# Performance work log

Measured on AMD Instinct MI355X. Metric: run time of the kernel, lower is better.

Reference implementation:

```python
import jax, jax.numpy as jnp
import numpy as np

DIM = 300
SCALES = (1, 2, 4, 10, 25)


def setup_inputs() -> dict:
    key = jax.random.key(0)
    k1, k2, k3 = jax.random.split(key, 3)
    N = 100000  # divisible by all scales -> rest == 0, matching the main path
    inputs_c_e = jax.random.normal(k1, (N, DIM), dtype=jnp.float32)
    Ws = jax.random.normal(k2, (len(SCALES), DIM, DIM), dtype=jnp.float32) * 0.05
    bs = jax.random.normal(k3, (len(SCALES), DIM), dtype=jnp.float32) * 0.05
    return {"inputs_c_e": inputs_c_e, "Ws": Ws, "bs": bs}


def _contract_expand(x, Ws, bs):
    # x: [N, DIM]; for each scale r: segment-sum groups of r rows, relu(Linear),
    # broadcast back (divided by r), then concat all scales along rows.
    N = x.shape[0]
    outs = []
    for i, r in enumerate(SCALES):
        groups = N // r
        rest = N - r * groups
        # sum over each full group of r consecutive rows -> [groups, DIM]
        sums = x[: r * groups].reshape(groups, r, DIM).sum(axis=1)
        if rest != 0:
            tail = x[r * groups :].sum(axis=0) * (r / rest)  # [DIM]
            sums = jnp.concatenate([sums, tail[None, :]], axis=0)
        # PyTorch Linear: y = s @ W.T + b, then relu, then divide by r
        h = jax.nn.relu(sums @ Ws[i].T + bs[i]) / r  # [groups(+1), DIM]
        expanded = jnp.repeat(h[:groups], r, axis=0)  # [r*groups, DIM]
        if rest != 0:
            expanded = jnp.concatenate(
                [expanded, jnp.broadcast_to(h[groups], (rest, DIM))], axis=0
            )
        outs.append(expanded)
    return jnp.concatenate(outs, axis=0)  # [5*N, DIM]


def reference(inputs_c_e, Ws, bs):
    return _contract_expand(inputs_c_e, Ws, bs)
```

## Files before the change

### kernel.cpp

```cpp
#include <hip/hip_runtime.h>
#include <hip/hip_bf16.h>

#define DIM 300

using shortx4 = __attribute__((ext_vector_type(4))) short;
using shortx8 = __attribute__((ext_vector_type(8))) short;
using floatx4 = __attribute__((ext_vector_type(4))) float;

__device__ __forceinline__ short f2bf(float f) {
  union { __hip_bfloat16 h; short s; } u;
  u.h = __float2bfloat16(f);
  return u.s;
}

__global__ void prep_w_kernel(const float* __restrict__ Ws, short* __restrict__ wsB) {
  int t = blockIdx.x * 256 + threadIdx.x;
  if (t >= 5 * 19 * 10 * 64) return;
  int fid = t >> 6, lane = t & 63;
  int s = fid / 190; int rem = fid - s * 190;
  int nt = rem / 10; int kk = rem - nt * 10;
  int n  = nt * 16 + (lane & 15);
  int k0 = kk * 32 + (lane >> 4) * 8;
  shortx8 v;
  #pragma unroll
  for (int j = 0; j < 8; ++j) {
    int k = k0 + j;
    float f = (n < DIM && k < DIM) ? Ws[s * (DIM * DIM) + n * DIM + k] : 0.0f;
    v[j] = f2bf(f);
  }
  *reinterpret_cast<shortx8*>(wsB + (size_t)fid * 512 + lane * 8) = v;
}

template <int R>
__device__ __forceinline__ void run_tile(
    const float* __restrict__ x, const float* __restrict__ bs,
    float* __restrict__ out, const short* __restrict__ wsB,
    int si, int tile, int N, short* A, float* bsh)
{
  const int tid = threadIdx.x;
  const int groups = N / R;
  const int g0 = tile * 64;
  int validM = groups - g0; if (validM > 64) validM = 64;

  for (int t = tid; t < 304; t += 256) bsh[t] = (t < DIM) ? bs[si * DIM + t] : 0.0f;

  for (int idx = tid; idx < 64 * 82; idx += 256) {
    int m  = idx / 82;
    int kv = idx - m * 82;
    float ax = 0.f, ay = 0.f, az = 0.f, aw = 0.f;
    if (kv < 75 && m < validM) {
      const float* p = x + ((size_t)(g0 + m) * R) * DIM + kv * 4;
      #pragma unroll
      for (int j = 0; j < R; ++j) {
        float4 v = *reinterpret_cast<const float4*>(p + j * DIM);
        ax += v.x; ay += v.y; az += v.z; aw += v.w;
      }
    }
    shortx4 h;
    h[0] = f2bf(ax); h[1] = f2bf(ay); h[2] = f2bf(az); h[3] = f2bf(aw);
    *reinterpret_cast<shortx4*>(&A[m * 328 + kv * 4]) = h;
  }
  __syncthreads();

  const int lane = tid & 63;
  const int wave = tid >> 6;
  const int lr   = lane & 15;
  const int quad = lane >> 4;
  const int wm   = wave * 16;

  shortx8 af[10];
  #pragma unroll
  for (int kk = 0; kk < 10; ++kk)
    af[kk] = *reinterpret_cast<const shortx8*>(&A[(wm + lr) * 328 + kk * 32 + quad * 8]);
  __syncthreads();

  short* Stage = A;
  const float inv_r = 1.0f / (float)R;
  const short* wb = wsB + (size_t)si * 190 * 512 + lane * 8;

  #pragma unroll 1
  for (int nt = 0; nt < 19; ++nt) {
    floatx4 acc = {0.f, 0.f, 0.f, 0.f};
    const short* wnt = wb + nt * 10 * 512;
    #pragma unroll
    for (int kk = 0; kk < 10; ++kk) {
      shortx8 bf = *reinterpret_cast<const shortx8*>(wnt + kk * 512);
      acc = __builtin_amdgcn_mfma_f32_16x16x32_bf16(af[kk], bf, acc, 0, 0, 0);
    }
    const int n = nt * 16 + lr;
    const float b = bsh[n];
    #pragma unroll
    for (int j = 0; j < 4; ++j) {
      float v = acc[j] + b;
      v = v > 0.f ? v * inv_r : 0.f;
      Stage[(wm + quad * 4 + j) * 312 + n] = f2bf(v);
    }
  }
  __syncthreads();

  float4* __restrict__ outv =
      reinterpret_cast<float4*>(out) + ((size_t)si * N + (size_t)g0 * R) * 75;
  const int total = validM * R * 75;
  for (int f = tid; f < total; f += 256) {
    int mr = f / 75;
    int c  = f - mr * 75;
    int sm = mr / R;
    int2 d = *reinterpret_cast<const int2*>(&Stage[sm * 312 + c * 4]);
    float4 o;
    o.x = __uint_as_float(((unsigned)d.x) << 16);
    o.y = __uint_as_float(((unsigned)d.x) & 0xffff0000u);
    o.z = __uint_as_float(((unsigned)d.y) << 16);
    o.w = __uint_as_float(((unsigned)d.y) & 0xffff0000u);
    outv[f] = o;
  }
}

__global__ __launch_bounds__(256) void ce_main_kernel(
    const float* __restrict__ x, const float* __restrict__ bs,
    float* __restrict__ out, const short* __restrict__ wsB,
    int N, int b0, int b1, int b2, int b3)
{
  __shared__ __align__(16) short A[64 * 328];
  __shared__ float bsh[304];
  const int bid = blockIdx.x;
  if (bid < b0)      run_tile<25>(x, bs, out, wsB, 4, bid,      N, A, bsh);
  else if (bid < b1) run_tile<10>(x, bs, out, wsB, 3, bid - b0, N, A, bsh);
  else if (bid < b2) run_tile<4> (x, bs, out, wsB, 2, bid - b1, N, A, bsh);
  else if (bid < b3) run_tile<2> (x, bs, out, wsB, 1, bid - b2, N, A, bsh);
  else               run_tile<1> (x, bs, out, wsB, 0, bid - b3, N, A, bsh);
}

extern "C" void kernel_launch(void* const* d_in, const int* in_sizes, int n_in,
                              void* d_out, int out_size, void* d_ws, size_t ws_size,
                              hipStream_t stream) {
  const float* x  = (const float*)d_in[0];
  const float* Ws = (const float*)d_in[1];
  const float* bs = (const float*)d_in[2];
  float* out = (float*)d_out;
  short* wsB = (short*)d_ws;

  const int N = in_sizes[0] / DIM;

  prep_w_kernel<<<(5 * 19 * 10 * 64 + 255) / 256, 256, 0, stream>>>(Ws, wsB);

  const int t25 = (N / 25 + 63) / 64;
  const int t10 = (N / 10 + 63) / 64;
  const int t4  = (N / 4  + 63) / 64;
  const int t2  = (N / 2  + 63) / 64;
  const int t1  = (N      + 63) / 64;
  const int b0 = t25;
  const int b1 = b0 + t10;
  const int b2 = b1 + t4;
  const int b3 = b2 + t2;
  const int total = b3 + t1;

  ce_main_kernel<<<total, 256, 0, stream>>>(x, bs, out, wsB, N, b0, b1, b2, b3);
}
```

Baseline: 800.2 us.

## Split segment-sum into separate kernel writing bf16 rows to workspace

Splits the fused kernel into a sum kernel, which reduces each group of rows to bf16 and writes it to a global workspace, and a GEMM+expand kernel that reads those bf16 rows straight into MFMA fragments. The second kernel needs only the staging buffer in LDS and requests 4 blocks per CU, so it can keep more blocks resident for the write-heavy expand phase. The sum loads also widen to 8 floats per thread. In exchange it adds an extra launch and a workspace round trip, and it falls back to the old kernel if the workspace is too small.

```diff
diff --git a/kernel.cpp b/kernel.cpp
--- a/kernel.cpp
+++ b/kernel.cpp
@@ -32,35 +32,65 @@
 }
 
 template <int R>
-__device__ __forceinline__ void run_tile(
-    const float* __restrict__ x, const float* __restrict__ bs,
-    float* __restrict__ out, const short* __restrict__ wsB,
-    int si, int tile, int N, short* A, float* bsh)
+__device__ __forceinline__ void sum_tile(
+    const float* __restrict__ x, short* __restrict__ Arow,
+    int tile, int bid, int N)
 {
   const int tid = threadIdx.x;
   const int groups = N / R;
   const int g0 = tile * 64;
   int validM = groups - g0; if (validM > 64) validM = 64;
-
-  for (int t = tid; t < 304; t += 256) bsh[t] = (t < DIM) ? bs[si * DIM + t] : 0.0f;
-
-  for (int idx = tid; idx < 64 * 82; idx += 256) {
-    int m  = idx / 82;
-    int kv = idx - m * 82;
-    float ax = 0.f, ay = 0.f, az = 0.f, aw = 0.f;
-    if (kv < 75 && m < validM) {
-      const float* p = x + ((size_t)(g0 + m) * R) * DIM + kv * 4;
+  short* dst = Arow + (size_t)bid * (64 * 320);
+
+  for (int idx = tid; idx < 64 * 40; idx += 256) {
+    int m  = idx / 40;
+    int ko = idx - m * 40;
+    float a0=0.f,a1=0.f,a2=0.f,a3=0.f,a4=0.f,a5=0.f,a6=0.f,a7=0.f;
+    if (m < validM) {
+      const float* p = x + ((size_t)(g0 + m) * R) * DIM + ko * 8;
+      const bool lo = (ko * 2     < 75);
+      const bool hi = (ko * 2 + 1 < 75);
       #pragma unroll
       for (int j = 0; j < R; ++j) {
-        float4 v = *reinterpret_cast<const float4*>(p + j * DIM);
-        ax += v.x; ay += v.y; az += v.z; aw += v.w;
+        if (lo) {
+          float4 v = *reinterpret_cast<const float4*>(p + j * DIM);
+          a0 += v.x; a1 += v.y; a2 += v.z; a3 += v.w;
+        }
+        if (hi) {
+          float4 v = *reinterpret_cast<const float4*>(p + j * DIM + 4);
+          a4 += v.x; a5 += v.y; a6 += v.z; a7 += v.w;
+        }
       }
     }
-    shortx4 h;
-    h[0] = f2bf(ax); h[1] = f2bf(ay); h[2] = f2bf(az); h[3] = f2bf(aw);
-    *reinterpret_cast<shortx4*>(&A[m * 328 + kv * 4]) = h;
-  }
-  __syncthreads();
+    shortx8 v;
+    v[0]=f2bf(a0); v[1]=f2bf(a1); v[2]=f2bf(a2); v[3]=f2bf(a3);
+    v[4]=f2bf(a4); v[5]=f2bf(a5); v[6]=f2bf(a6); v[7]=f2bf(a7);
+    *reinterpret_cast<shortx8*>(dst + m * 320 + ko * 8) = v;
+  }
+}
+
+__global__ __launch_bounds__(256) void sum_kernel(
+    const float* __restrict__ x, short* __restrict__ Arow,
+    int N, int b0, int b1, int b2, int b3)
+{
+  const int bid = blockIdx.x;
+  if (bid < b0)      sum_tile<25>(x, Arow, bid,      bid, N);
+  else if (bid < b1) sum_tile<10>(x, Arow, bid - b0, bid, N);
+  else if (bid < b2) sum_tile<4> (x, Arow, bid - b1, bid, N);
+  else if (bid < b3) sum_tile<2> (x, Arow, bid - b2, bid, N);
+  else               sum_tile<1> (x, Arow, bid - b3, bid, N);
+}
+
+template <int R>
+__device__ __forceinline__ void run_tile2(
+    const float* __restrict__ bs, float* __restrict__ out,
+    const short* __restrict__ wsB, const short* __restrict__ Arow,
+    int si, int tile, int bid, int N, short* Stage)
+{
+  const int tid = threadIdx.x;
+  const int groups = N / R;
+  const int g0 = tile * 64;
+  int validM = groups - g0; if (validM > 64) validM = 64;
 
   const int lane = tid & 63;
   const int wave = tid >> 6;
@@ -68,13 +98,12 @@
   const int quad = lane >> 4;
   const int wm   = wave * 16;
 
+  const short* arow = Arow + ((size_t)bid * 64 + wm + lr) * 320 + quad * 8;
   shortx8 af[10];
   #pragma unroll
   for (int kk = 0; kk < 10; ++kk)
-    af[kk] = *reinterpret_cast<const shortx8*>(&A[(wm + lr) * 328 + kk * 32 + quad * 8]);
-  __syncthreads();
-
-  short* Stage = A;
+    af[kk] = *reinterpret_cast<const shortx8*>(arow + kk * 32);
+
   const float inv_r = 1.0f / (float)R;
   const short* wb = wsB + (size_t)si * 190 * 512 + lane * 8;
 
@@ -88,7 +117,7 @@
       acc = __builtin_amdgcn_mfma_f32_16x16x32_bf16(af[kk], bf, acc, 0, 0, 0);
     }
     const int n = nt * 16 + lr;
-    const float b = bsh[n];
+    const float b = (n < DIM) ? bs[si * DIM + n] : 0.0f;
     #pragma unroll
     for (int j = 0; j < 4; ++j) {
       float v = acc[j] + b;
@@ -115,6 +144,104 @@
   }
 }
 
+__global__ __launch_bounds__(256, 4) void ce_main2_kernel(
+    const float* __restrict__ bs, float* __restrict__ out,
+    const short* __restrict__ wsB, const short* __restrict__ Arow,
+    int N, int b0, int b1, int b2, int b3)
+{
+  __shared__ __align__(16) short Stage[64 * 312];
+  const int bid = blockIdx.x;
+  if (bid < b0)      run_tile2<25>(bs, out, wsB, Arow, 4, bid,      bid, N, Stage);
+  else if (bid < b1) run_tile2<10>(bs, out, wsB, Arow, 3, bid - b0, bid, N, Stage);
+  else if (bid < b2) run_tile2<4> (bs, out, wsB, Arow, 2, bid - b1, bid, N, Stage);
+  else if (bid < b3) run_tile2<2> (bs, out, wsB, Arow, 1, bid - b2, bid, N, Stage);
+  else               run_tile2<1> (bs, out, wsB, Arow, 0, bid - b3, bid, N, Stage);
+}
+
+template <int R>
+__device__ __forceinline__ void run_tile(
+    const float* __restrict__ x, const float* __restrict__ bs,
+    float* __restrict__ out, const short* __restrict__ wsB,
+    int si, int tile, int N, short* A, float* bsh)
+{
+  const int tid = threadIdx.x;
+  const int groups = N / R;
+  const int g0 = tile * 64;
+  int validM = groups - g0; if (validM > 64) validM = 64;
+
+  for (int t = tid; t < 304; t += 256) bsh[t] = (t < DIM) ? bs[si * DIM + t] : 0.0f;
+
+  for (int idx = tid; idx < 64 * 82; idx += 256) {
+    int m  = idx / 82;
+    int kv = idx - m * 82;
+    float ax = 0.f, ay = 0.f, az = 0.f, aw = 0.f;
+    if (kv < 75 && m < validM) {
+      const float* p = x + ((size_t)(g0 + m) * R) * DIM + kv * 4;
+      #pragma unroll
+      for (int j = 0; j < R; ++j) {
+        float4 v = *reinterpret_cast<const float4*>(p + j * DIM);
+        ax += v.x; ay += v.y; az += v.z; aw += v.w;
+      }
+    }
+    shortx4 h;
+    h[0] = f2bf(ax); h[1] = f2bf(ay); h[2] = f2bf(az); h[3] = f2bf(aw);
+    *reinterpret_cast<shortx4*>(&A[m * 328 + kv * 4]) = h;
+  }
+  __syncthreads();
+
+  const int lane = tid & 63;
+  const int wave = tid >> 6;
+  const int lr   = lane & 15;
+  const int quad = lane >> 4;
+  const int wm   = wave * 16;
+
+  shortx8 af[10];
+  #pragma unroll
+  for (int kk = 0; kk < 10; ++kk)
+    af[kk] = *reinterpret_cast<const shortx8*>(&A[(wm + lr) * 328 + kk * 32 + quad * 8]);
+  __syncthreads();
+
+  short* Stage = A;
+  const float inv_r = 1.0f / (float)R;
+  const short* wb = wsB + (size_t)si * 190 * 512 + lane * 8;
+
+  #pragma unroll 1
+  for (int nt = 0; nt < 19; ++nt) {
+    floatx4 acc = {0.f, 0.f, 0.f, 0.f};
+    const short* wnt = wb + nt * 10 * 512;
+    #pragma unroll
+    for (int kk = 0; kk < 10; ++kk) {
+      shortx8 bf = *reinterpret_cast<const shortx8*>(wnt + kk * 512);
+      acc = __builtin_amdgcn_mfma_f32_16x16x32_bf16(af[kk], bf, acc, 0, 0, 0);
+    }
+    const int n = nt * 16 + lr;
+    const float b = bsh[n];
+    #pragma unroll
+    for (int j = 0; j < 4; ++j) {
+      float v = acc[j] + b;
+      v = v > 0.f ? v * inv_r : 0.f;
+      Stage[(wm + quad * 4 + j) * 312 + n] = f2bf(v);
+    }
+  }
+  __syncthreads();
+
+  float4* __restrict__ outv =
+      reinterpret_cast<float4*>(out) + ((size_t)si * N + (size_t)g0 * R) * 75;
+  const int total = validM * R * 75;
+  for (int f = tid; f < total; f += 256) {
+    int mr = f / 75;
+    int c  = f - mr * 75;
+    int sm = mr / R;
+    int2 d = *reinterpret_cast<const int2*>(&Stage[sm * 312 + c * 4]);
+    float4 o;
+    o.x = __uint_as_float(((unsigned)d.x) << 16);
+    o.y = __uint_as_float(((unsigned)d.x) & 0xffff0000u);
+    o.z = __uint_as_float(((unsigned)d.y) << 16);
+    o.w = __uint_as_float(((unsigned)d.y) & 0xffff0000u);
+    outv[f] = o;
+  }
+}
+
 __global__ __launch_bounds__(256) void ce_main_kernel(
     const float* __restrict__ x, const float* __restrict__ bs,
     float* __restrict__ out, const short* __restrict__ wsB,
@@ -154,5 +281,14 @@
   const int b3 = b2 + t2;
   const int total = b3 + t1;
 
-  ce_main_kernel<<<total, 256, 0, stream>>>(x, bs, out, wsB, N, b0, b1, b2, b3);
-}
+  const size_t wsB_bytes = 972800;
+  const size_t arow_bytes = (size_t)total * 64 * 320 * sizeof(short);
+
+  if (ws_size >= wsB_bytes + arow_bytes) {
+    short* Arow = wsB + wsB_bytes / sizeof(short);
+    sum_kernel<<<total, 256, 0, stream>>>(x, Arow, N, b0, b1, b2, b3);
+    ce_main2_kernel<<<total, 256, 0, stream>>>(bs, out, wsB, Arow, N, b0, b1, b2, b3);
+  } else {
+    ce_main_kernel<<<total, 256, 0, stream>>>(x, bs, out, wsB, N, b0, b1, b2, b3);
+  }
+}
```

New measurement: 916.1 us. 14.5% more time.

## Make each wave own its 16 rows end to end and drop block barriers

Applied to the files above, without the earlier changes.

Each wave now loads and sums only its own 16 rows of A, reads its MFMA fragments, stages its output and writes it out with no __syncthreads. A row stride of 320 with an XOR swizzle is meant to avoid LDS bank conflicts. Bias now comes straight from global memory, and launch bounds ask for 4 blocks per CU. The aim is to remove block-wide barrier stalls and raise occupancy. The wave-private buffer relies on in-wave ordering of LDS writes and reads, and 16-byte loads per lane change how global accesses coalesce.

```diff
diff --git a/kernel.cpp b/kernel.cpp
--- a/kernel.cpp
+++ b/kernel.cpp
@@ -3,7 +3,6 @@
 
 #define DIM 300
 
-using shortx4 = __attribute__((ext_vector_type(4))) short;
 using shortx8 = __attribute__((ext_vector_type(8))) short;
 using floatx4 = __attribute__((ext_vector_type(4))) float;
 
@@ -35,46 +34,52 @@
 __device__ __forceinline__ void run_tile(
     const float* __restrict__ x, const float* __restrict__ bs,
     float* __restrict__ out, const short* __restrict__ wsB,
-    int si, int tile, int N, short* A, float* bsh)
+    int si, int tile, int N, short* A)
 {
-  const int tid = threadIdx.x;
+  const int tid  = threadIdx.x;
+  const int lane = tid & 63;
+  const int wave = tid >> 6;
+  const int wm   = wave * 16;
   const int groups = N / R;
   const int g0 = tile * 64;
   int validM = groups - g0; if (validM > 64) validM = 64;
 
-  for (int t = tid; t < 304; t += 256) bsh[t] = (t < DIM) ? bs[si * DIM + t] : 0.0f;
-
-  for (int idx = tid; idx < 64 * 82; idx += 256) {
-    int m  = idx / 82;
-    int kv = idx - m * 82;
-    float ax = 0.f, ay = 0.f, az = 0.f, aw = 0.f;
-    if (kv < 75 && m < validM) {
-      const float* p = x + ((size_t)(g0 + m) * R) * DIM + kv * 4;
+  for (int idx = lane; idx < 640; idx += 64) {
+    int ml = idx / 40;
+    int ko = idx - ml * 40;
+    int m  = wm + ml;
+    float a0=0.f,a1=0.f,a2=0.f,a3=0.f,a4=0.f,a5=0.f,a6=0.f,a7=0.f;
+    if (m < validM) {
+      const float* p = x + ((size_t)(g0 + m) * R) * DIM + ko * 8;
+      const bool lo = (ko <= 37);
+      const bool hi = (ko <= 36);
       #pragma unroll
       for (int j = 0; j < R; ++j) {
-        float4 v = *reinterpret_cast<const float4*>(p + j * DIM);
-        ax += v.x; ay += v.y; az += v.z; aw += v.w;
+        if (lo) {
+          float4 v = *reinterpret_cast<const float4*>(p + j * DIM);
+          a0 += v.x; a1 += v.y; a2 += v.z; a3 += v.w;
+        }
+        if (hi) {
+          float4 v = *reinterpret_cast<const float4*>(p + j * DIM + 4);
+          a4 += v.x; a5 += v.y; a6 += v.z; a7 += v.w;
+        }
       }
     }
-    shortx4 h;
-    h[0] = f2bf(ax); h[1] = f2bf(ay); h[2] = f2bf(az); h[3] = f2bf(aw);
-    *reinterpret_cast<shortx4*>(&A[m * 328 + kv * 4]) = h;
+    shortx8 v8;
+    v8[0]=f2bf(a0); v8[1]=f2bf(a1); v8[2]=f2bf(a2); v8[3]=f2bf(a3);
+    v8[4]=f2bf(a4); v8[5]=f2bf(a5); v8[6]=f2bf(a6); v8[7]=f2bf(a7);
+    *reinterpret_cast<shortx8*>(&A[m * 320 + ((ko ^ (ml & 7)) * 8)]) = v8;
   }
-  __syncthreads();
 
-  const int lane = tid & 63;
-  const int wave = tid >> 6;
   const int lr   = lane & 15;
   const int quad = lane >> 4;
-  const int wm   = wave * 16;
-
   shortx8 af[10];
   #pragma unroll
-  for (int kk = 0; kk < 10; ++kk)
-    af[kk] = *reinterpret_cast<const shortx8*>(&A[(wm + lr) * 328 + kk * 32 + quad * 8]);
-  __syncthreads();
+  for (int kk = 0; kk < 10; ++kk) {
+    int oct = (kk * 4 + quad) ^ (lr & 7);
+    af[kk] = *reinterpret_cast<const shortx8*>(&A[(wm + lr) * 320 + oct * 8]);
+  }
 
-  short* Stage = A;
   const float inv_r = 1.0f / (float)R;
   const short* wb = wsB + (size_t)si * 190 * 512 + lane * 8;
 
@@ -88,24 +93,25 @@
       acc = __builtin_amdgcn_mfma_f32_16x16x32_bf16(af[kk], bf, acc, 0, 0, 0);
     }
     const int n = nt * 16 + lr;
-    const float b = bsh[n];
+    const float b = (n < DIM) ? bs[si * DIM + n] : 0.0f;
     #pragma unroll
     for (int j = 0; j < 4; ++j) {
       float v = acc[j] + b;
       v = v > 0.f ? v * inv_r : 0.f;
-      Stage[(wm + quad * 4 + j) * 312 + n] = f2bf(v);
+      A[(wm + quad * 4 + j) * 320 + n] = f2bf(v);
     }
   }
-  __syncthreads();
 
+  int vmw = validM - wm; if (vmw > 16) vmw = 16; if (vmw < 0) vmw = 0;
   float4* __restrict__ outv =
-      reinterpret_cast<float4*>(out) + ((size_t)si * N + (size_t)g0 * R) * 75;
-  const int total = validM * R * 75;
-  for (int f = tid; f < total; f += 256) {
+      reinterpret_cast<float4*>(out) + ((size_t)si * N + (size_t)(g0 + wm) * R) * 75;
+  const short* src = A + wm * 320;
+  const int total = vmw * R * 75;
+  for (int f = lane; f < total; f += 64) {
     int mr = f / 75;
     int c  = f - mr * 75;
     int sm = mr / R;
-    int2 d = *reinterpret_cast<const int2*>(&Stage[sm * 312 + c * 4]);
+    int2 d = *reinterpret_cast<const int2*>(&src[sm * 320 + c * 4]);
     float4 o;
     o.x = __uint_as_float(((unsigned)d.x) << 16);
     o.y = __uint_as_float(((unsigned)d.x) & 0xffff0000u);
@@ -115,19 +121,18 @@
   }
 }
 
-__global__ __launch_bounds__(256) void ce_main_kernel(
+__global__ __launch_bounds__(256, 4) void ce_main_kernel(
     const float* __restrict__ x, const float* __restrict__ bs,
     float* __restrict__ out, const short* __restrict__ wsB,
     int N, int b0, int b1, int b2, int b3)
 {
-  __shared__ __align__(16) short A[64 * 328];
-  __shared__ float bsh[304];
+  __shared__ __align__(16) short A[64 * 320];
   const int bid = blockIdx.x;
-  if (bid < b0)      run_tile<25>(x, bs, out, wsB, 4, bid,      N, A, bsh);
-  else if (bid < b1) run_tile<10>(x, bs, out, wsB, 3, bid - b0, N, A, bsh);
-  else if (bid < b2) run_tile<4> (x, bs, out, wsB, 2, bid - b1, N, A, bsh);
-  else if (bid < b3) run_tile<2> (x, bs, out, wsB, 1, bid - b2, N, A, bsh);
-  else               run_tile<1> (x, bs, out, wsB, 0, bid - b3, N, A, bsh);
+  if (bid < b0)      run_tile<25>(x, bs, out, wsB, 4, bid,      N, A);
+  else if (bid < b1) run_tile<10>(x, bs, out, wsB, 3, bid - b0, N, A);
+  else if (bid < b2) run_tile<4> (x, bs, out, wsB, 2, bid - b1, N, A);
+  else if (bid < b3) run_tile<2> (x, bs, out, wsB, 1, bid - b2, N, A);
+  else               run_tile<1> (x, bs, out, wsB, 0, bid - b3, N, A);
 }
 
 extern "C" void kernel_launch(void* const* d_in, const int* in_sizes, int n_in,
```

Result: slower. 837.9 us (+4.7%).
